# Kernel tuning notes

Hardware: AMD Instinct MI355X
Metric: run time of the kernel (lower is better)

## Reference

```python
import jax, jax.numpy as jnp
import numpy as np

N, K = 512, 17
W, H = 48, 64          # heatmap_size = [W, H]
LOSS_WEIGHT = 1.0
EPS = 1e-9


def setup_inputs() -> dict:
    key = jax.random.key(0)
    k1, k2, k3 = jax.random.split(key, 3)
    pred = jax.random.uniform(k1, (N, K, 2), dtype=jnp.float32)           # normalized kpt coords in [0,1)
    sigma = jax.random.uniform(k2, (N, K, 2), dtype=jnp.float32) * 3.0 + 1.0  # realistic gaussian widths [1,4)
    teacher_hm = jax.random.uniform(k3, (N, K, H, W), dtype=jnp.float32)
    target_weight = jnp.ones((N, K, 1), dtype=jnp.float32)                # joints_3d_visible[..., :1]
    return {"pred": pred, "sigma": sigma, "teacher_hm": teacher_hm,
            "target_weight": target_weight}


def reference(pred, sigma, teacher_hm, target_weight):
    # MSRA unbiased encoding (vectorized branch), gaussian_mode='s2'
    mu_x = pred[..., 0] * W                      # [N,K]
    mu_y = pred[..., 1] * H
    sx = sigma[..., 0]
    sy = sigma[..., 1]

    # visibility mask: gaussian bbox must intersect the heatmap
    mask = ((mu_x - 3.0 * sx < W) & (mu_y - 3.0 * sy < H) &
            (mu_x + 3.0 * sx + 1.0 >= 0) & (mu_y + 3.0 * sy + 1.0 >= 0)
            ).astype(jnp.float32)                # [N,K]
    tw = target_weight[..., 0] * mask            # [N,K]

    x = jnp.arange(W, dtype=jnp.float32)         # [W]
    y = jnp.arange(H, dtype=jnp.float32)         # [H]
    dx2 = (x[None, None, None, :] - mu_x[..., None, None]) ** 2 / (sx[..., None, None] ** 2 + EPS)
    dy2 = (y[None, None, :, None] - mu_y[..., None, None]) ** 2 / (sy[..., None, None] ** 2 + EPS)
    g = jnp.exp(-0.5 * (dx2 + dy2))              # [N,K,H,W]
    target = g * mask[..., None, None]

    # JointsMSELoss with use_target_weight: mean over joints of MSE(w*pred, w*gt)
    w = tw[..., None, None]                      # [N,K,1,1]
    loss = jnp.mean((w * (target - teacher_hm)) ** 2) * LOSS_WEIGHT
    return loss
```

## Files before the change

kernel.cpp:

```cpp
#include <hip/hip_runtime.h>

#define NN 512
#define KK 17
#define WW 48
#define HH 64
#define HW (WW * HH)
#define NK (NN * KK)
#define IPB 4
#define NBLK (NK / IPB)


__global__ __launch_bounds__(256, 4) void reg2hm_partial_kernel(
    const float* __restrict__ pred,
    const float* __restrict__ sigma,
    const float* __restrict__ teacher,
    const float* __restrict__ twgt,
    float* __restrict__ ws)
{
    __shared__ float4 ex4[IPB][WW / 4];
    __shared__ float  ey4[IPB][HH];
    __shared__ float  sw[IPB];
    __shared__ float  wave_sums[4];

    const int b   = blockIdx.x;
    const int nk0 = b * IPB;
    const int t   = threadIdx.x;

    if (t < IPB) {
        const int nk = nk0 + t;
        const float mu_x = pred[nk * 2 + 0] * (float)WW;
        const float mu_y = pred[nk * 2 + 1] * (float)HH;
        const float sx   = sigma[nk * 2 + 0];
        const float sy   = sigma[nk * 2 + 1];
        const bool m = (mu_x - 3.0f * sx < (float)WW) &&
                       (mu_y - 3.0f * sy < (float)HH) &&
                       (mu_x + 3.0f * sx + 1.0f >= 0.0f) &&
                       (mu_y + 3.0f * sy + 1.0f >= 0.0f);
        sw[t] = twgt[nk] * (m ? 1.0f : 0.0f);
    }

    float* exf = (float*)ex4;
    for (int i = t; i < IPB * (WW + HH); i += 256) {
        const int item = i / (WW + HH);
        const int r    = i - item * (WW + HH);
        const int nk   = nk0 + item;
        if (r < WW) {
            const float mu = pred[nk * 2 + 0] * (float)WW;
            const float s  = sigma[nk * 2 + 0];
            const float d  = (float)r - mu;
            exf[item * WW + r] = __expf(-d * d * (0.5f / (s * s + 1e-9f)));
        } else {
            const float mu = pred[nk * 2 + 1] * (float)HH;
            const float s  = sigma[nk * 2 + 1];
            const float d  = (float)(r - WW) - mu;
            ey4[item][r - WW] = __expf(-d * d * (0.5f / (s * s + 1e-9f)));
        }
    }
    __syncthreads();

    float4 tv[IPB * 3];
#pragma unroll
    for (int item = 0; item < IPB; ++item) {
        const float4* tp = (const float4*)(teacher + (size_t)(nk0 + item) * HW);
#pragma unroll
        for (int j = 0; j < 3; ++j)
            tv[item * 3 + j] = tp[t + j * 256];
    }

    float total = 0.0f;
#pragma unroll
    for (int item = 0; item < IPB; ++item) {
        float acc = 0.0f;
#pragma unroll
        for (int j = 0; j < 3; ++j) {
            const int i = t + j * 256;
            const int h = i / 12;
            const int s = i - h * 12;
            const float4 e  = ex4[item][s];
            const float  ey = ey4[item][h];
            const float4 v  = tv[item * 3 + j];
            const float d0 = e.x * ey - v.x;
            const float d1 = e.y * ey - v.y;
            const float d2 = e.z * ey - v.z;
            const float d3 = e.w * ey - v.w;
            acc += d0 * d0 + d1 * d1 + d2 * d2 + d3 * d3;
        }
        total += sw[item] * sw[item] * acc;
    }

#pragma unroll
    for (int off = 32; off > 0; off >>= 1)
        total += __shfl_down(total, off, 64);

    const int wave = t >> 6;
    const int lane = t & 63;
    if (lane == 0) wave_sums[wave] = total;
    __syncthreads();

    if (t == 0)
        ws[b] = wave_sums[0] + wave_sums[1] + wave_sums[2] + wave_sums[3];
}

__global__ __launch_bounds__(256) void reg2hm_final_kernel(
    const float* __restrict__ ws, float* __restrict__ out)
{
    __shared__ float wave_sums[4];
    const int t = threadIdx.x;
    float sum = 0.0f;
    for (int i = t; i < NBLK; i += 256) sum += ws[i];
#pragma unroll
    for (int off = 32; off > 0; off >>= 1)
        sum += __shfl_down(sum, off, 64);
    const int wave = t >> 6;
    const int lane = t & 63;
    if (lane == 0) wave_sums[wave] = sum;
    __syncthreads();
    if (t == 0) {
        const float total = wave_sums[0] + wave_sums[1] + wave_sums[2] + wave_sums[3];
        out[0] = total * (1.0f / ((float)NN * KK * HW));
    }
}

extern "C" void kernel_launch(void* const* d_in, const int* in_sizes, int n_in,
                              void* d_out, int out_size, void* d_ws, size_t ws_size,
                              hipStream_t stream) {
    const float* pred    = (const float*)d_in[0];
    const float* sigma   = (const float*)d_in[1];
    const float* teacher = (const float*)d_in[2];
    const float* twgt    = (const float*)d_in[3];
    float* out = (float*)d_out;
    float* ws  = (float*)d_ws;

    reg2hm_partial_kernel<<<NBLK, 256, 0, stream>>>(pred, sigma, teacher, twgt, ws);
    reg2hm_final_kernel<<<1, 256, 0, stream>>>(ws, out);
}
```

Before: 166.0 us.

## Process all joints of one sample per block with register prefetch pipeline

Each block now handles all 17 keypoints of one sample instead of 4 keypoints. A one-step software prefetch loads the next heatmap while the current one is reduced, which keeps register use low. This also cuts the block count and partial sums, but with only 512 blocks and 3 loads in flight per thread, memory-level parallelism and occupancy may drop.

```diff
diff --git a/kernel.cpp b/kernel.cpp
--- a/kernel.cpp
+++ b/kernel.cpp
@@ -6,27 +6,25 @@
 #define HH 64
 #define HW (WW * HH)
 #define NK (NN * KK)
-#define IPB 4
-#define NBLK (NK / IPB)
 
 
-__global__ __launch_bounds__(256, 4) void reg2hm_partial_kernel(
+__global__ __launch_bounds__(256) void reg2hm_partial_kernel(
     const float* __restrict__ pred,
     const float* __restrict__ sigma,
     const float* __restrict__ teacher,
     const float* __restrict__ twgt,
     float* __restrict__ ws)
 {
-    __shared__ float4 ex4[IPB][WW / 4];
-    __shared__ float  ey4[IPB][HH];
-    __shared__ float  sw[IPB];
+    __shared__ float4 ex4[KK][WW / 4];
+    __shared__ float  eys[KK][HH];
+    __shared__ float  sw[KK];
     __shared__ float  wave_sums[4];
 
-    const int b   = blockIdx.x;
-    const int nk0 = b * IPB;
+    const int n   = blockIdx.x;
+    const int nk0 = n * KK;
     const int t   = threadIdx.x;
 
-    if (t < IPB) {
+    if (t < KK) {
         const int nk = nk0 + t;
         const float mu_x = pred[nk * 2 + 0] * (float)WW;
         const float mu_y = pred[nk * 2 + 1] * (float)HH;
@@ -40,7 +38,7 @@
     }
 
     float* exf = (float*)ex4;
-    for (int i = t; i < IPB * (WW + HH); i += 256) {
+    for (int i = t; i < KK * (WW + HH); i += 256) {
         const int item = i / (WW + HH);
         const int r    = i - item * (WW + HH);
         const int nk   = nk0 + item;
@@ -53,39 +51,54 @@
             const float mu = pred[nk * 2 + 1] * (float)HH;
             const float s  = sigma[nk * 2 + 1];
             const float d  = (float)(r - WW) - mu;
-            ey4[item][r - WW] = __expf(-d * d * (0.5f / (s * s + 1e-9f)));
+            eys[item][r - WW] = __expf(-d * d * (0.5f / (s * s + 1e-9f)));
         }
     }
     __syncthreads();
 
-    float4 tv[IPB * 3];
-#pragma unroll
-    for (int item = 0; item < IPB; ++item) {
-        const float4* tp = (const float4*)(teacher + (size_t)(nk0 + item) * HW);
-#pragma unroll
-        for (int j = 0; j < 3; ++j)
-            tv[item * 3 + j] = tp[t + j * 256];
-    }
+    const int i0 = t;
+    const int i1 = t + 256;
+    const int i2 = t + 512;
+    const int h0 = i0 / 12, s0 = i0 - h0 * 12;
+    const int h1 = i1 / 12, s1 = i1 - h1 * 12;
+    const int h2 = i2 / 12, s2 = i2 - h2 * 12;
 
+    const float4* tp = (const float4*)(teacher + (size_t)nk0 * HW);
+
+    float4 c0 = tp[i0], c1 = tp[i1], c2 = tp[i2];
     float total = 0.0f;
-#pragma unroll
-    for (int item = 0; item < IPB; ++item) {
+#pragma unroll 1
+    for (int item = 0; item < KK; ++item) {
+        float4 n0, n1, n2;
+        if (item < KK - 1) {
+            const float4* np_ = tp + (item + 1) * (HW / 4);
+            n0 = np_[i0]; n1 = np_[i1]; n2 = np_[i2];
+        }
+        const float4 e0 = ex4[item][s0];
+        const float4 e1 = ex4[item][s1];
+        const float4 e2 = ex4[item][s2];
+        const float  y0 = eys[item][h0];
+        const float  y1 = eys[item][h1];
+        const float  y2 = eys[item][h2];
+
         float acc = 0.0f;
-#pragma unroll
-        for (int j = 0; j < 3; ++j) {
-            const int i = t + j * 256;
-            const int h = i / 12;
-            const int s = i - h * 12;
-            const float4 e  = ex4[item][s];
-            const float  ey = ey4[item][h];
-            const float4 v  = tv[item * 3 + j];
-            const float d0 = e.x * ey - v.x;
-            const float d1 = e.y * ey - v.y;
-            const float d2 = e.z * ey - v.z;
-            const float d3 = e.w * ey - v.w;
+        {
+            const float d0 = e0.x * y0 - c0.x, d1 = e0.y * y0 - c0.y;
+            const float d2 = e0.z * y0 - c0.z, d3 = e0.w * y0 - c0.w;
+            acc += d0 * d0 + d1 * d1 + d2 * d2 + d3 * d3;
+        }
+        {
+            const float d0 = e1.x * y1 - c1.x, d1 = e1.y * y1 - c1.y;
+            const float d2 = e1.z * y1 - c1.z, d3 = e1.w * y1 - c1.w;
+            acc += d0 * d0 + d1 * d1 + d2 * d2 + d3 * d3;
+        }
+        {
+            const float d0 = e2.x * y2 - c2.x, d1 = e2.y * y2 - c2.y;
+            const float d2 = e2.z * y2 - c2.z, d3 = e2.w * y2 - c2.w;
             acc += d0 * d0 + d1 * d1 + d2 * d2 + d3 * d3;
         }
         total += sw[item] * sw[item] * acc;
+        c0 = n0; c1 = n1; c2 = n2;
     }
 
 #pragma unroll
@@ -98,7 +111,7 @@
     __syncthreads();
 
     if (t == 0)
-        ws[b] = wave_sums[0] + wave_sums[1] + wave_sums[2] + wave_sums[3];
+        ws[n] = wave_sums[0] + wave_sums[1] + wave_sums[2] + wave_sums[3];
 }
 
 __global__ __launch_bounds__(256) void reg2hm_final_kernel(
@@ -107,7 +120,7 @@
     __shared__ float wave_sums[4];
     const int t = threadIdx.x;
     float sum = 0.0f;
-    for (int i = t; i < NBLK; i += 256) sum += ws[i];
+    for (int i = t; i < NN; i += 256) sum += ws[i];
 #pragma unroll
     for (int off = 32; off > 0; off >>= 1)
         sum += __shfl_down(sum, off, 64);
@@ -131,6 +144,6 @@
     float* out = (float*)d_out;
     float* ws  = (float*)d_ws;
 
-    reg2hm_partial_kernel<<<NBLK, 256, 0, stream>>>(pred, sigma, teacher, twgt, ws);
+    reg2hm_partial_kernel<<<NN, 256, 0, stream>>>(pred, sigma, teacher, twgt, ws);
     reg2hm_final_kernel<<<1, 256, 0, stream>>>(ws, out);
 }
```

After: 167.0 us. No clear change (+0.6%).
